# Optimization experiments

Measured on AMD Instinct MI355X. Metric: run time of the kernel, lower is better.

Reference implementation:

```python
import jax, jax.numpy as jnp
import numpy as np
from jax import lax


def _conv_layer(x, K, k, stride, pad):
    """Faithful reimplementation of the custom Conv2d, including its two quirks:
    1) weight/input flatten-order mismatch: K.reshape(k*k*cin, cout) pairs flat
       index m (decoded as kh,kw,cin for K) against x flattened as (cin,kh,kw),
       so the effective conv weight is K.reshape(-1,cout).reshape(cin,k,k,cout).
    2) the python loop range(0, padd-k, stride) misses the last valid position
       whenever (padd-k) is divisible by stride, leaving last row/col zero.
    """
    B, cin, s_in, _ = x.shape
    cout = K.shape[-1]
    out_size = (s_in + 2 * pad - k) // stride + 1
    padd = s_in + 2 * pad
    n_loop = -(-(padd - k) // stride)  # = len(range(0, padd-k, stride))
    xp = jnp.pad(x, ((0, 0), (0, 0), (pad, pad), (pad, pad))) if pad > 0 else x
    # effective weight honoring the flatten-order mismatch: (cin, kh, kw, cout)
    W = K.reshape(-1, cout).reshape(cin, k, k, cout)
    y = lax.conv_general_dilated(
        xp, W, window_strides=(stride, stride), padding='VALID',
        dimension_numbers=('NCHW', 'IHWO', 'NCHW'))
    n = min(n_loop, out_size)
    out = jnp.zeros((B, cout, out_size, out_size), x.dtype)
    out = out.at[:, :, :n, :n].set(y[:, :, :n, :n])
    return out


def setup_inputs() -> dict:
    key = jax.random.key(0)
    ks = jax.random.split(key, 9)
    NUM_CLASSES = 10
    B = 8192

    def kinit(k_, shape):
        fan_in = shape[1] * int(np.prod(shape[2:]))  # torch fan_in for 4D
        bound = float(np.sqrt(6.0 / fan_in))
        return jax.random.uniform(k_, shape, jnp.float32, -bound, bound)

    x = jax.random.normal(ks[0], (B, 3, 28, 28), jnp.float32)
    K1 = kinit(ks[1], (5, 5, 3, 8))
    K2 = kinit(ks[2], (3, 3, 8, 16))
    K3 = kinit(ks[3], (3, 3, 16, 16))
    K4 = kinit(ks[4], (3, 3, 16, 16))
    K5 = kinit(ks[5], (3, 3, 16, 16))
    K6 = kinit(ks[6], (5, 5, 16, 32))
    fc_in = 6 * 6 * 32  # 1152
    bw = float(np.sqrt(1.0 / fc_in))
    Wfc = jax.random.uniform(ks[7], (NUM_CLASSES, fc_in), jnp.float32, -bw, bw)
    bfc = jax.random.uniform(ks[8], (NUM_CLASSES,), jnp.float32, -bw, bw)
    return {"x": x, "K1": K1, "K2": K2, "K3": K3, "K4": K4, "K5": K5,
            "K6": K6, "Wfc": Wfc, "bfc": bfc}


def reference(x, K1, K2, K3, K4, K5, K6, Wfc, bfc):
    h = jax.nn.relu(_conv_layer(x, K1, 5, 2, 1))   # (B,8,13,13)
    h = jax.nn.relu(_conv_layer(h, K2, 3, 1, 1))   # (B,16,13,13), last row/col zero
    h = jax.nn.relu(_conv_layer(h, K3, 3, 1, 1))
    h = jax.nn.relu(_conv_layer(h, K4, 3, 1, 1))
    h = jax.nn.relu(_conv_layer(h, K5, 3, 1, 1))
    h = _conv_layer(h, K6, 5, 2, 1)                # (B,32,6,6), last row/col zero
    flat = h.reshape(h.shape[0], -1)               # (B,1152)
    logits = flat @ Wfc.T + bfc
    return jax.nn.softmax(logits, axis=1)
```

## Files before the change

### kernel.cpp

```cpp
#include <hip/hip_runtime.h>
#include <hip/hip_bf16.h>
#include <math.h>

#define TPB 256

typedef __attribute__((ext_vector_type(8))) short short8;
typedef __attribute__((ext_vector_type(4))) float f32x4;
typedef unsigned short u16;

__device__ __forceinline__ f32x4 MFMA(short8 a, short8 b, f32x4 c) {
    return __builtin_amdgcn_mfma_f32_16x16x32_bf16(a, b, c, 0, 0, 0);
}
__device__ __forceinline__ u16 f2bf(float f) {
    unsigned int u = __builtin_bit_cast(unsigned int, f);
    u += 0x7FFFu + ((u >> 16) & 1u);
    return (u16)(u >> 16);
}
__device__ __forceinline__ u16 f2bf_hw(float f) {
    __hip_bfloat16 b = __float2bfloat16(f);
    return __builtin_bit_cast(u16, b);
}
__device__ __forceinline__ float bf2f(u16 h) {
    unsigned int u = ((unsigned int)h) << 16;
    return __builtin_bit_cast(float, u);
}

extern "C" __global__ void prep_w(const float* __restrict__ K1, const float* __restrict__ K2,
                                  const float* __restrict__ K3, const float* __restrict__ K4,
                                  const float* __restrict__ K5, const float* __restrict__ K6,
                                  short8* __restrict__ W)
{
    const int slot = blockIdx.x * blockDim.x + threadIdx.x;
    if (slot >= 6144) return;
    const int lane = slot & 63;
    const int ent  = slot >> 6;
    const int o    = lane & 15;
    const int lhi  = lane >> 4;
    float w[8];
    int hl;
    if (ent < 6) {
        const int s = ent >> 1; hl = ent & 1;
        const int t = s * 4 + lhi;
#pragma unroll
        for (int j = 0; j < 8; j++)
            w[j] = (t < 9) ? K2[(j * 9 + t) * 16 + o] : 0.f;
    } else if (ent < 36) {
        const int e  = ent - 6;
        const float* Kg = (e < 10) ? K3 : (e < 20) ? K4 : K5;
        const int el = e % 10;
        const int s  = el >> 1; hl = el & 1;
        const int chalf = (lhi & 1) * 8;
        const int t = 2 * s + (lhi >> 1);
#pragma unroll
        for (int j = 0; j < 8; j++)
            w[j] = (t < 9) ? Kg[((chalf + j) * 9 + t) * 16 + o] : 0.f;
    } else if (ent < 88) {
        const int e = ent - 36;
        const int s = e >> 2; hl = (e >> 1) & 1;
        const int nh = e & 1;
        const int chalf = (lhi & 1) * 8;
        const int t  = 2 * s + (lhi >> 1);
        const int oo = nh * 16 + o;
#pragma unroll
        for (int j = 0; j < 8; j++)
            w[j] = (t < 25) ? K6[((chalf + j) * 25 + t) * 32 + oo] : 0.f;
    } else {
        const int e = ent - 88;
        const int s = e >> 1; hl = e & 1;
        const int g  = s * 4 + lhi;
        const int gc = g > 14 ? 14 : g;
        const int c  = (gc * 52) >> 8;
        const int kh = gc - 5 * c;
#pragma unroll
        for (int j = 0; j < 8; j++)
            w[j] = (g < 15 && o < 8 && j < 5) ? K1[(c * 25 + kh * 5 + j) * 8 + o] : 0.f;
    }
    short8 v;
#pragma unroll
    for (int j = 0; j < 8; j++) {
        const u16 h = f2bf(w[j]);
        v[j] = hl ? (short)f2bf(w[j] - bf2f(h)) : (short)h;
    }
    W[slot] = v;
}


__device__ __forceinline__ void conv8(const u16* __restrict__ s0,
                                      u16* __restrict__ d0,
                                      const short8* __restrict__ Wt,
                                      int wave, int lane, int rot)
{
    const int o   = lane & 15;
    const int lhi = lane >> 4;
    short8 Bhi[3], Blo[3];
#pragma unroll
    for (int s = 0; s < 3; s++) {
        Bhi[s] = Wt[(s * 2 + 0) * 64 + lane];
        Blo[s] = Wt[(s * 2 + 1) * 64 + lane];
    }
    const u16* sl = s0 + 3600;
    const int r0 = lane & 15;

    auto tile = [&](int m) {
        const int p  = m * 16 + r0;
        const int ip = (p * 683) >> 13;
        const int jp = p - 12 * ip;
        f32x4 acc = {0.f, 0.f, 0.f, 0.f};
#pragma unroll
        for (int s = 0; s < 3; s++) {
            const int t  = s * 4 + lhi;
            const int tt = t > 8 ? 8 : t;
            const int kh = (tt * 11) >> 5;
            const int kw = tt - 3 * kh;
            const int px = (ip + kh) * 15 + (jp + kw);
            const short8 Ahi = *(const short8*)(s0 + px * 8);
            const short8 Alo = *(const short8*)(sl + px * 8);
            acc = MFMA(Ahi, Bhi[s], acc);
            acc = MFMA(Alo, Bhi[s], acc);
            acc = MFMA(Ahi, Blo[s], acc);
        }
        const int p0 = m * 16 + lhi * 4;
#pragma unroll
        for (int r = 0; r < 4; r++) {
            const int pp = p0 + r;
            const int ii = (pp * 683) >> 13;
            const int jj = pp - 12 * ii;
            const float v = fmaxf(acc[r], 0.f);
            const u16 h = f2bf_hw(v);
            const int px2 = (ii + 1) * 15 + (jj + 1);
            const int da  = (o >> 3) * 1800 + px2 * 8 + (o & 7);
            d0[da]        = h;
            d0[da + 3600] = f2bf_hw(v - bf2f(h));
        }
    };
    const int m0 = (wave + rot) & 3;
    tile(m0);
    tile(m0 + 4);
    if (m0 == 0) tile(8);
}

__device__ __forceinline__ void conv16(const u16* __restrict__ s0,
                                       u16* __restrict__ d0,
                                       const short8* __restrict__ Wt,
                                       int wave, int lane, int rot)
{
    const int o    = lane & 15;
    const int lhi  = lane >> 4;
    const int hsel = lhi & 1;
    const int tsel = lhi >> 1;
    short8 Bhi[5], Blo[5];
#pragma unroll
    for (int s = 0; s < 5; s++) {
        Bhi[s] = Wt[(s * 2 + 0) * 64 + lane];
        Blo[s] = Wt[(s * 2 + 1) * 64 + lane];
    }
    const u16* sh = s0 + hsel * 1800;
    const u16* sl = sh + 3600;
    const int r0 = lane & 15;

    auto tile = [&](int m) {
        const int p  = m * 16 + r0;
        const int ip = (p * 683) >> 13;
        const int jp = p - 12 * ip;
        f32x4 acc = {0.f, 0.f, 0.f, 0.f};
#pragma unroll
        for (int s = 0; s < 5; s++) {
            const int t  = 2 * s + tsel;
            const int tt = t > 8 ? 8 : t;
            const int kh = (tt * 11) >> 5;
            const int kw = tt - 3 * kh;
            const int px = (ip + kh) * 15 + (jp + kw);
            const short8 Ahi = *(const short8*)(sh + px * 8);
            const short8 Alo = *(const short8*)(sl + px * 8);
            acc = MFMA(Ahi, Bhi[s], acc);
            acc = MFMA(Alo, Bhi[s], acc);
            acc = MFMA(Ahi, Blo[s], acc);
        }
        const int p0 = m * 16 + lhi * 4;
#pragma unroll
        for (int r = 0; r < 4; r++) {
            const int pp = p0 + r;
            const int ii = (pp * 683) >> 13;
            const int jj = pp - 12 * ii;
            const float v = fmaxf(acc[r], 0.f);
            const u16 h = f2bf_hw(v);
            const int px2 = (ii + 1) * 15 + (jj + 1);
            const int da  = (o >> 3) * 1800 + px2 * 8 + (o & 7);
            d0[da]        = h;
            d0[da + 3600] = f2bf_hw(v - bf2f(h));
        }
    };
    const int m0 = (wave + rot) & 3;
    tile(m0);
    tile(m0 + 4);
    if (m0 == 0) tile(8);
}

extern "C" __global__ void __launch_bounds__(TPB)
cnn_fused(const float* __restrict__ xg,
          const float* __restrict__ Wfc, const float* __restrict__ bfc,
          const short8* __restrict__ W, float* __restrict__ out)
{
    __shared__ __align__(16) unsigned char smem[28864];
    u16*   const Ah   = (u16*)smem;
    u16*   const Bh   = (u16*)(smem + 14400);
    u16*   const Sh   = (u16*)(smem + 14400);
    float* const sF   = (float*)(smem + 14400);
    float* const sLog = (float*)(smem + 28800);
    uint4* const z4   = (uint4*)smem;
    const uint4 Z = {0u, 0u, 0u, 0u};

    const int tid  = threadIdx.x;
    const int lane = tid & 63;
    const int wave = tid >> 6;
    const int img  = blockIdx.x;

    for (int i = tid; i < 1804; i += TPB) z4[i] = Z;
    __syncthreads();

    const float4* xi4 = (const float4*)(xg + (size_t)img * 2352);
    for (int i4 = tid; i4 < 588; i4 += TPB) {
        const float4 v = xi4[i4];
        const int c = i4 / 196;
        const int rem = i4 - c * 196;
        const int r = rem / 7;
        const int q = rem - r * 7;
        const int ad = c * 960 + (r + 1) * 32 + q * 4 + 1;
        const float vv[4] = {v.x, v.y, v.z, v.w};
#pragma unroll
        for (int e = 0; e < 4; e++) {
            const u16 h = f2bf_hw(vv[e]);
            Sh[ad + e]        = h;
            Sh[ad + e + 2880] = f2bf_hw(vv[e] - bf2f(h));
        }
    }
    __syncthreads();

    {
        const short8* Wt1 = W + 5632;
        const int o   = lane & 15;
        const int lhi = lane >> 4;
        short8 B1h[4], B1l[4];
#pragma unroll
        for (int s = 0; s < 4; s++) {
            B1h[s] = Wt1[(s * 2 + 0) * 64 + lane];
            B1l[s] = Wt1[(s * 2 + 1) * 64 + lane];
        }
        const u16* slo = Sh + 2880;
        for (int m = wave; m < 11; m += 4) {
            const int p  = m * 16 + o;
            const int pc = p > 168 ? 168 : p;
            const int i = (pc * 316) >> 12;
            const int j = pc - 13 * i;
            f32x4 acc = {0.f, 0.f, 0.f, 0.f};
#pragma unroll
            for (int s = 0; s < 4; s++) {
                const int g  = s * 4 + lhi;
                const int gc = g > 14 ? 14 : g;
                const int c  = (gc * 52) >> 8;
                const int kh = gc - 5 * c;
                const int ad = c * 960 + (2 * i + kh) * 32 + 2 * j;
                const short8 Ahi = *(const short8*)(Sh + ad);
                const short8 Alo = *(const short8*)(slo + ad);
                acc = MFMA(Ahi, B1h[s], acc);
                acc = MFMA(Alo, B1h[s], acc);
                acc = MFMA(Ahi, B1l[s], acc);
            }
#pragma unroll
            for (int r = 0; r < 4; r++) {
                const int pp = m * 16 + lhi * 4 + r;
                if (pp < 169 && o < 8) {
                    const int ii = (pp * 316) >> 12;
                    const int jj = pp - 13 * ii;
                    const float v = fmaxf(acc[r], 0.f);
                    const u16 h = f2bf_hw(v);
                    const int da = ((ii + 1) * 15 + (jj + 1)) * 8 + o;
                    Ah[da]        = h;
                    Ah[da + 3600] = f2bf_hw(v - bf2f(h));
                }
            }
        }
    }
    __syncthreads();

    for (int i = tid; i < 900; i += TPB) z4[900 + i] = Z;
    __syncthreads();

    conv8(Ah, Bh, W, wave, lane, 0);
    __syncthreads();
    conv16(Bh, Ah, W + 384, wave, lane, 1);
    __syncthreads();
    conv16(Ah, Bh, W + 1024, wave, lane, 2);
    __syncthreads();
    conv16(Bh, Ah, W + 1664, wave, lane, 3);
    __syncthreads();

    for (int i = tid; i < 288; i += TPB) z4[900 + i] = Z;
    __syncthreads();

    if (wave < 4) {
        const short8* Wt6 = W + 2304;
        const int mt   = wave >> 1;
        const int nh   = wave & 1;
        const int lhi  = lane >> 4;
        const int hsel = lhi & 1;
        const int tsel = lhi >> 1;
        const int o    = nh * 16 + (lane & 15);
        const int pr = mt * 16 + (lane & 15);
        const int pe = pr < 25 ? pr : 0;
        const int ia = (pe * 52) >> 8;
        const int ja = pe - 5 * ia;
        const u16* sh = Ah + hsel * 1800;
        const u16* sl = sh + 3600;
        f32x4 acc = {0.f, 0.f, 0.f, 0.f};
#pragma unroll 4
        for (int s = 0; s < 13; s++) {
            const int t  = 2 * s + tsel;
            const int tt = t > 24 ? 24 : t;
            const int kh = (tt * 52) >> 8;
            const int kw = tt - 5 * kh;
            const int px = (2 * ia + kh) * 15 + (2 * ja + kw);
            const short8 Ahi = *(const short8*)(sh + px * 8);
            const short8 Alo = *(const short8*)(sl + px * 8);
            const short8 Bh2 = Wt6[((s * 2 + 0) * 2 + nh) * 64 + lane];
            const short8 Bl2 = Wt6[((s * 2 + 1) * 2 + nh) * 64 + lane];
            acc = MFMA(Ahi, Bh2, acc);
            acc = MFMA(Alo, Bh2, acc);
            acc = MFMA(Ahi, Bl2, acc);
        }
        const int p0 = mt * 16 + lhi * 4;
#pragma unroll
        for (int r = 0; r < 4; r++) {
            const int pp = p0 + r;
            if (pp < 25) {
                const int ii = (pp * 52) >> 8;
                const int jj = pp - 5 * ii;
                sF[o * 36 + ii * 6 + jj] = acc[r];
            }
        }
    }
    __syncthreads();

    if (tid < 160) {
        const int c = tid >> 4;
        const int l = tid & 15;
        const float4* fv = (const float4*)(sF + l * 72);
        const float4* wv = (const float4*)(Wfc + c * 1152 + l * 72);
        float p = 0.f;
#pragma unroll
        for (int m = 0; m < 18; m++) {
            const float4 a = fv[m];
            const float4 b = wv[m];
            p = fmaf(a.x, b.x, p);
            p = fmaf(a.y, b.y, p);
            p = fmaf(a.z, b.z, p);
            p = fmaf(a.w, b.w, p);
        }
        p += __shfl_down(p, 8, 16);
        p += __shfl_down(p, 4, 16);
        p += __shfl_down(p, 2, 16);
        p += __shfl_down(p, 1, 16);
        if (l == 0) sLog[c] = p + bfc[c];
    }
    __syncthreads();

    if (tid < 10) {
        float mx = sLog[0];
#pragma unroll
        for (int k = 1; k < 10; k++) mx = fmaxf(mx, sLog[k]);
        float s = 0.f;
#pragma unroll
        for (int k = 0; k < 10; k++) s += expf(sLog[k] - mx);
        out[(size_t)img * 10 + tid] = expf(sLog[tid] - mx) / s;
    }
}

extern "C" void kernel_launch(void* const* d_in, const int* in_sizes, int n_in,
                              void* d_out, int out_size, void* d_ws, size_t ws_size,
                              hipStream_t stream) {
    const float* x   = (const float*)d_in[0];
    const float* K1  = (const float*)d_in[1];
    const float* K2  = (const float*)d_in[2];
    const float* K3  = (const float*)d_in[3];
    const float* K4  = (const float*)d_in[4];
    const float* K5  = (const float*)d_in[5];
    const float* K6  = (const float*)d_in[6];
    const float* Wfc = (const float*)d_in[7];
    const float* bfc = (const float*)d_in[8];
    float* out = (float*)d_out;
    short8* W = (short8*)d_ws;

    prep_w<<<24, 256, 0, stream>>>(K1, K2, K3, K4, K5, K6, W);

    const int B = in_sizes[0] / 2352;
    cnn_fused<<<B, TPB, 0, stream>>>(x, Wfc, bfc, W, out);
}
```

Baseline: 204.9 us.

## Use five waves per block and zero only halo borders instead of full buffers

```diff
diff --git a/kernel.cpp b/kernel.cpp
--- a/kernel.cpp
+++ b/kernel.cpp
@@ -2,7 +2,7 @@
 #include <hip/hip_bf16.h>
 #include <math.h>
 
-#define TPB 256
+#define TPB 320
 
 typedef __attribute__((ext_vector_type(8))) short short8;
 typedef __attribute__((ext_vector_type(4))) float f32x4;
@@ -133,10 +133,10 @@
             d0[da + 3600] = f2bf_hw(v - bf2f(h));
         }
     };
-    const int m0 = (wave + rot) & 3;
+    int m0 = wave + rot;
+    if (m0 >= 5) m0 -= 5;
     tile(m0);
-    tile(m0 + 4);
-    if (m0 == 0) tile(8);
+    if (m0 <= 3) tile(m0 + 5);
 }
 
 __device__ __forceinline__ void conv16(const u16* __restrict__ s0,
@@ -190,10 +190,10 @@
             d0[da + 3600] = f2bf_hw(v - bf2f(h));
         }
     };
-    const int m0 = (wave + rot) & 3;
+    int m0 = wave + rot;
+    if (m0 >= 5) m0 -= 5;
     tile(m0);
-    tile(m0 + 4);
-    if (m0 == 0) tile(8);
+    if (m0 <= 3) tile(m0 + 5);
 }
 
 extern "C" __global__ void __launch_bounds__(TPB)
@@ -247,7 +247,7 @@
             B1l[s] = Wt1[(s * 2 + 1) * 64 + lane];
         }
         const u16* slo = Sh + 2880;
-        for (int m = wave; m < 11; m += 4) {
+        for (int m = wave; m < 11; m += 5) {
             const int p  = m * 16 + o;
             const int pc = p > 168 ? 168 : p;
             const int i = (pc * 316) >> 12;
@@ -283,21 +283,35 @@
     }
     __syncthreads();
 
-    for (int i = tid; i < 900; i += TPB) z4[900 + i] = Z;
-    __syncthreads();
-
     conv8(Ah, Bh, W, wave, lane, 0);
-    __syncthreads();
+    if (tid < 208) {
+        const int pl = tid / 52, e = tid - pl * 52;
+        const int px = (e < 14) ? e
+                     : (e < 28) ? 195 + (e - 14)
+                     : (e < 40) ? (e - 27) * 15
+                                : (e - 39) * 15 + 13;
+        z4[900 + pl * 225 + px] = Z;
+    }
+    __syncthreads();
+
     conv16(Bh, Ah, W + 384, wave, lane, 1);
-    __syncthreads();
+    if (tid < 108) {
+        const int pl = tid / 27, e = tid - pl * 27;
+        const int px = (e < 14) ? 195 + e : (e - 14) * 15 + 13;
+        z4[pl * 225 + px] = Z;
+    }
+    __syncthreads();
+
     conv16(Ah, Bh, W + 1024, wave, lane, 2);
     __syncthreads();
     conv16(Bh, Ah, W + 1664, wave, lane, 3);
     __syncthreads();
 
-    for (int i = tid; i < 288; i += TPB) z4[900 + i] = Z;
-    __syncthreads();
-
+    for (int i = tid; i < 352; i += TPB) {
+        const int o = i / 11, k = i - o * 11;
+        const int slot = (k < 6) ? o * 36 + 30 + k : o * 36 + (k - 6) * 6 + 5;
+        sF[slot] = 0.f;
+    }
     if (wave < 4) {
         const short8* Wt6 = W + 2304;
         const int mt   = wave >> 1;
```

After: 251.9 us. 1.23x slower.
